# Performance work log

Hardware: AMD Instinct MI355X
Metric: run time of the kernel (lower is better)

## Reference

```python
import jax, jax.numpy as jnp
import numpy as np

B, S, I, H = 16, 4096, 256, 256
H_CYCLES, L_CYCLES = 2, 3


def setup_inputs() -> dict:
    key = jax.random.key(0)
    ks = jax.random.split(key, 18)
    g = lambda k, shape, s=0.05: jax.random.normal(k, shape, dtype=jnp.float32) * s
    return {
        "x": g(ks[0], (B, S, I), 1.0),
        "h0": jnp.zeros((1, B, H), jnp.float32),
        # GRU (PyTorch layout: rows ordered [reset, update, new])
        "gru_w_ih": g(ks[1], (3 * H, I)),
        "gru_w_hh": g(ks[2], (3 * H, H)),
        "gru_b_ih": g(ks[3], (3 * H,)),
        "gru_b_hh": g(ks[4], (3 * H,)),
        # L refine cell
        "Lg_w": g(ks[5], (H, 2 * H)), "Lg_b": g(ks[6], (H,)),
        "Lt_w": g(ks[7], (H, 2 * H)), "Lt_b": g(ks[8], (H,)),
        "Lu_w": g(ks[9], (H, H)),     "Lu_b": g(ks[10], (H,)),
        # H refine cell
        "Hg_w": g(ks[11], (H, 2 * H)), "Hg_b": g(ks[12], (H,)),
        "Ht_w": g(ks[13], (H, 2 * H)), "Ht_b": g(ks[14], (H,)),
        "Hu_w": g(ks[15], (H, H)),     "Hu_b": g(ks[16], (H,)),
    }


def _refine_cell(prev, hid, gw, gb, tw, tb, uw, ub):
    c = jnp.concatenate([prev, hid], axis=-1)            # (B, 2H)
    gate = jax.nn.sigmoid(c @ gw.T + gb)
    refinement = jnp.tanh(c @ tw.T + tb)
    out = gate * refinement + (1.0 - gate) * prev
    new_hid = jnp.tanh(out @ uw.T + ub)
    return out, new_hid


def reference(x, h0, gru_w_ih, gru_w_hh, gru_b_ih, gru_b_hh,
              Lg_w, Lg_b, Lt_w, Lt_b, Lu_w, Lu_b,
              Hg_w, Hg_b, Ht_w, Ht_b, Hu_w, Hu_b):
    # ---- GRU (single layer, batch_first), PyTorch gate equations ----
    x_proj = x @ gru_w_ih.T + gru_b_ih                   # (B, S, 3H)

    def gru_step(h, xp):
        hp = h @ gru_w_hh.T + gru_b_hh                   # (B, 3H)
        xr, xz, xn = jnp.split(xp, 3, axis=-1)
        hr, hz, hn = jnp.split(hp, 3, axis=-1)
        r = jax.nn.sigmoid(xr + hr)
        z = jax.nn.sigmoid(xz + hz)
        n = jnp.tanh(xn + r * hn)
        h_new = (1.0 - z) * n + z * h
        return h_new, h_new

    h_last, base_out = jax.lax.scan(gru_step, h0[0], x_proj.transpose(1, 0, 2))
    # base_out: (S, B, H)

    # ---- hierarchical recursive refinement; zH/zL persist across t ----
    def refine_step(carry, out_t):
        zH, zL = carry
        o = out_t
        for _ in range(H_CYCLES):
            for _ in range(L_CYCLES):
                o, zL = _refine_cell(o, zH, Lg_w, Lg_b, Lt_w, Lt_b, Lu_w, Lu_b)
            o, zH = _refine_cell(o, zL, Hg_w, Hg_b, Ht_w, Ht_b, Hu_w, Hu_b)
        return (zH, zL), o

    z0 = jnp.zeros((x.shape[0], H), x.dtype)
    _, refined = jax.lax.scan(refine_step, (z0, z0), base_out)  # (S, B, H)
    output = refined.transpose(1, 0, 2)                  # (B, S, H)
    return output, h_last[None]                          # hidden: (1, B, H)
```

## Files before the change

### kernel.cpp

```cpp
#include <hip/hip_runtime.h>
#include <math.h>


#define NB   16
#define SEQ  4096
#define TEAMS 8
#define WPT  32
#define BPT  2
#define NTH  256

typedef unsigned long long u64;
typedef unsigned u32x4 __attribute__((ext_vector_type(4)));

__device__ __forceinline__ float fexp(float v){ return __builtin_amdgcn_exp2f(v*1.44269504089f); }
__device__ __forceinline__ float sigf(float v){ return __builtin_amdgcn_rcpf(1.f + fexp(-v)); }
__device__ __forceinline__ float ftanh(float v){ return 2.f*sigf(2.f*v) - 1.f; }

__device__ __forceinline__ void swpw(u64* p, u64 v){
  (void)__hip_atomic_exchange(p, v, __ATOMIC_RELAXED, __HIP_MEMORY_SCOPE_AGENT);
}
__device__ __forceinline__ u64 ldw(const u64* p){
  return __hip_atomic_load(p, __ATOMIC_RELAXED, __HIP_MEMORY_SCOPE_AGENT);
}

typedef _Float16 h2f __attribute__((ext_vector_type(2)));
typedef __fp16   h2p __attribute__((ext_vector_type(2)));
union H2U { h2f f; h2p p; unsigned u; };
__device__ __forceinline__ unsigned pk2(float lo, float hi){
  H2U t; t.p = __builtin_amdgcn_cvt_pkrtz(lo, hi); return t.u;
}
__device__ __forceinline__ float2 upk2(unsigned w){
  H2U t; t.u = w; float2 r; r.x = (float)t.f.x; r.y = (float)t.f.y; return r;
}
__device__ __forceinline__ u64 packh(float lo, float hi, unsigned tag){
  return ((u64)tag<<32) | (u64)pk2(lo, hi);
}

__device__ __forceinline__ void poll2x(const u64* p, unsigned tag,
                                       unsigned &lo0, unsigned &lo1){
  u32x4 v;
  for(;;){
    asm volatile("global_load_dwordx4 %0, %1, off sc0 sc1\n\ts_waitcnt vmcnt(0)"
                 : "=&v"(v) : "v"(p) : "memory");
    if (v.y >= tag && v.w >= tag) break;
    __builtin_amdgcn_s_sleep(1);
  }
  lo0 = v.x; lo1 = v.z;
}

#define WGBAR() asm volatile("s_waitcnt lgkmcnt(0)\n\ts_barrier" ::: "memory")

extern "C" __global__ __launch_bounds__(NTH, 1)
void trm_kernel(const float* __restrict__ x,   const float* __restrict__ h0,
                const float* __restrict__ wih, const float* __restrict__ whh,
                const float* __restrict__ bih, const float* __restrict__ bhh,
                const float* __restrict__ Lgw, const float* __restrict__ Lgb,
                const float* __restrict__ Ltw, const float* __restrict__ Ltb,
                const float* __restrict__ Luw, const float* __restrict__ Lub,
                const float* __restrict__ Hgw, const float* __restrict__ Hgb,
                const float* __restrict__ Htw, const float* __restrict__ Htb,
                const float* __restrict__ Huw, const float* __restrict__ Hub,
                float* __restrict__ out, u64* __restrict__ act_base)
{
  const int team = blockIdx.x & (TEAMS-1);
  const int j    = blockIdx.x / TEAMS;
  const int tid  = threadIdx.x;

  __shared__ float wgRZ[16][520];
  __shared__ float wgX[8][264];
  __shared__ float wgN[8][264];
  __shared__ float wclG[8][520], wclT[8][520];
  __shared__ float wchG[8][520], wchT[8][520];
  __shared__ float wul[8][264],  wuh[8][264];
  __shared__ float xst [BPT][256];
  __shared__ float st_o [BPT][256];
  __shared__ float st_zh[BPT][256];
  __shared__ float st_zl[BPT][256];
  __shared__ float st_h [BPT][256];
  __shared__ float exvA[16][2], exvC[16][2], exvD[16][2];
  __shared__ float bR[8],bZ[8],bX[8],bN[8],bCLg[8],bCLt[8],bCHg[8],bCHt[8],bUL[8],bUH[8];

  {
    const int k = tid;
    for (int r=0;r<8;r++){
      const int nr = j*8+r;
      wgRZ[r][k]       = wih[(size_t)nr*256+k];
      wgRZ[r][256+k]   = whh[(size_t)nr*256+k];
      wgRZ[8+r][k]     = wih[(size_t)(256+nr)*256+k];
      wgRZ[8+r][256+k] = whh[(size_t)(256+nr)*256+k];
      wgX[r][k] = wih[(size_t)(512+nr)*256+k];
      wgN[r][k] = whh[(size_t)(512+nr)*256+k];
      wclG[r][k] = Lgw[(size_t)nr*512+k];  wclG[r][256+k] = Lgw[(size_t)nr*512+256+k];
      wclT[r][k] = Ltw[(size_t)nr*512+k];  wclT[r][256+k] = Ltw[(size_t)nr*512+256+k];
      wchG[r][k] = Hgw[(size_t)nr*512+k];  wchG[r][256+k] = Hgw[(size_t)nr*512+256+k];
      wchT[r][k] = Htw[(size_t)nr*512+k];  wchT[r][256+k] = Htw[(size_t)nr*512+256+k];
      wul[r][k] = Luw[(size_t)nr*256+k];
      wuh[r][k] = Huw[(size_t)nr*256+k];
    }
    if (tid<8){
      const int nr = j*8+tid;
      bR[tid]  = bih[nr]     + bhh[nr];
      bZ[tid]  = bih[256+nr] + bhh[256+nr];
      bX[tid]  = bih[512+nr];
      bN[tid]  = bhh[512+nr];
      bCLg[tid]= Lgb[nr];  bCLt[tid]= Ltb[nr];
      bCHg[tid]= Hgb[nr];  bCHt[tid]= Htb[nr];
      bUL[tid] = Lub[nr];  bUH[tid] = Hub[nr];
    }
    st_h[0][tid]  = h0[(team*BPT+0)*256+tid];
    st_h[1][tid]  = h0[(team*BPT+1)*256+tid];
    st_o[0][tid]  = 0.f;  st_o[1][tid]  = 0.f;
    st_zh[0][tid] = 0.f;  st_zh[1][tid] = 0.f;
    st_zl[0][tid] = 0.f;  st_zl[1][tid] = 0.f;
    xst[0][tid] = x[((size_t)(team*BPT+0)*SEQ + 0)*256 + tid];
    xst[1][tid] = x[((size_t)(team*BPT+1)*SEQ + 0)*256 + tid];
  }
  __syncthreads();

  u64* actT = act_base + (size_t)team*4096;
  u64* gb   = actT + 2048;
  unsigned kst = 0;
  const bool wr0 = (j == 0);

  auto gru_produce = [&](int step){
    const unsigned gt = (unsigned)step + 1u;
    u64* g = gb + (size_t)(step & 1)*512;
    const int u = tid>>4, kk = tid&15, r = u&7;
    {
      const float* wr = wgRZ[u];
      float a0=0.f, a1=0.f;
      #pragma unroll
      for (int i=0;i<16;i++){
        const float w = wr[kk+16*i];
        a0 += w*xst[0][kk+16*i];
        a1 += w*xst[1][kk+16*i];
      }
      #pragma unroll
      for (int i=0;i<16;i++){
        const float w = wr[256+kk+16*i];
        a0 += w*st_h[0][kk+16*i];
        a1 += w*st_h[1][kk+16*i];
      }
      a0 += __shfl_xor(a0,1); a0 += __shfl_xor(a0,2); a0 += __shfl_xor(a0,4); a0 += __shfl_xor(a0,8);
      a1 += __shfl_xor(a1,1); a1 += __shfl_xor(a1,2); a1 += __shfl_xor(a1,4); a1 += __shfl_xor(a1,8);
      if (kk==0){ exvC[u][0] = a0; exvC[u][1] = a1; }
    }
    {
      const bool isH = (u>=8);
      const float* wr = isH? wgN[r] : wgX[r];
      float (*src)[256] = isH? st_h : xst;
      float a0=0.f, a1=0.f;
      #pragma unroll
      for (int i=0;i<16;i++){
        const float w = wr[kk+16*i];
        a0 += w*src[0][kk+16*i];
        a1 += w*src[1][kk+16*i];
      }
      a0 += __shfl_xor(a0,1); a0 += __shfl_xor(a0,2); a0 += __shfl_xor(a0,4); a0 += __shfl_xor(a0,8);
      a1 += __shfl_xor(a1,1); a1 += __shfl_xor(a1,2); a1 += __shfl_xor(a1,4); a1 += __shfl_xor(a1,8);
      if (kk==0){ exvD[u][0] = a0; exvD[u][1] = a1; }
    }
    WGBAR();
    if (tid < 16){
      const int b = tid&1, rr = tid>>1;
      const float pr = exvC[rr][b]   + bR[rr];
      const float pz = exvC[8+rr][b] + bZ[rr];
      const float xn = exvD[rr][b]   + bX[rr];
      const float hn = exvD[8+rr][b] + bN[rr];
      const float rg = sigf(pr);
      const float zg = sigf(pz);
      const float ng = ftanh(xn + rg*hn);
      swpw(&g[(size_t)(j*8+rr)*2 + b], packh(ng, zg, gt));
    }
  };

  auto cstage = [&](float (*WG)[520], float (*WT)[520], float* bG, float* bT,
                    float (*hid)[256], bool wout, bool pg, int tt){
    const unsigned tag = kst + 1u;
    u64* buf = actT + (kst & 1u)*1024;
    WGBAR();
    const int u = tid>>4, kk = tid&15, r = u&7;
    const bool isT = (u>=8);
    const float* wr = isT? WT[r] : WG[r];
    float a0=0.f, a1=0.f;
    #pragma unroll
    for (int i=0;i<16;i++){
      const float w = wr[kk+16*i];
      a0 += w*st_o[0][kk+16*i];
      a1 += w*st_o[1][kk+16*i];
    }
    #pragma unroll
    for (int i=0;i<16;i++){
      const float w = wr[256+kk+16*i];
      a0 += w*hid[0][kk+16*i];
      a1 += w*hid[1][kk+16*i];
    }
    a0 += __shfl_xor(a0,1); a0 += __shfl_xor(a0,2); a0 += __shfl_xor(a0,4); a0 += __shfl_xor(a0,8);
    a1 += __shfl_xor(a1,1); a1 += __shfl_xor(a1,2); a1 += __shfl_xor(a1,4); a1 += __shfl_xor(a1,8);
    if (kk==0){ exvA[u][0] = a0; exvA[u][1] = a1; }
    WGBAR();
    if (tid < 16){
      const int b = tid&1, rr = tid>>1;
      const float g = sigf (exvA[rr][b]   + bG[rr]);
      const float T = ftanh(exvA[8+rr][b] + bT[rr]);
      swpw(&buf[(size_t)(j*8+rr)*2 + b], packh(g, T, tag));
    }
    if (pg) gru_produce(tt+1);
    unsigned lo0, lo1;
    poll2x(&buf[2*tid], tag, lo0, lo1);
    const float2 gt0 = upk2(lo0);
    const float2 gt1 = upk2(lo1);
    const float o0 = gt0.x*gt0.y + (1.f-gt0.x)*st_o[0][tid];
    const float o1 = gt1.x*gt1.y + (1.f-gt1.x)*st_o[1][tid];
    st_o[0][tid] = o0;
    st_o[1][tid] = o1;
    if (wout && wr0){
      out[((size_t)(team*BPT+0)*SEQ + tt)*256 + tid] = o0;
      out[((size_t)(team*BPT+1)*SEQ + tt)*256 + tid] = o1;
    }
    kst++;
  };

  auto ustage = [&](float (*W)[264], float* bU, float (*dst)[256]){
    const unsigned tag = kst + 1u;
    u64* buf = actT + (kst & 1u)*1024;
    WGBAR();
    const int u = tid>>5, kk = tid&31;
    const float* wr = W[u];
    float a0=0.f, a1=0.f;
    #pragma unroll
    for (int i=0;i<8;i++){
      const float w = wr[kk+32*i];
      a0 += w*st_o[0][kk+32*i];
      a1 += w*st_o[1][kk+32*i];
    }
    a0 += __shfl_xor(a0,1); a0 += __shfl_xor(a0,2); a0 += __shfl_xor(a0,4); a0 += __shfl_xor(a0,8); a0 += __shfl_xor(a0,16);
    a1 += __shfl_xor(a1,1); a1 += __shfl_xor(a1,2); a1 += __shfl_xor(a1,4); a1 += __shfl_xor(a1,8); a1 += __shfl_xor(a1,16);
    if (kk==0){ exvA[u][0] = a0; exvA[u][1] = a1; }
    WGBAR();
    if (tid < 8){
      const float v0 = ftanh(exvA[tid][0] + bU[tid]);
      const float v1 = ftanh(exvA[tid][1] + bU[tid]);
      swpw(&buf[j*8 + tid], packh(v0, v1, tag));
    }
    u64 w0;
    for(;;){
      w0 = ldw(&buf[tid]);
      if ((unsigned)(w0>>32) >= tag) break;
      __builtin_amdgcn_s_sleep(1);
    }
    const float2 v = upk2((unsigned)w0);
    dst[0][tid] = v.x;
    dst[1][tid] = v.y;
    kst++;
  };

  float px0 = x[((size_t)(team*BPT+0)*SEQ + 1)*256 + tid];
  float px1 = x[((size_t)(team*BPT+1)*SEQ + 1)*256 + tid];
  gru_produce(0);

  #pragma unroll 1
  for (int t=0; t<SEQ; ++t){
    {
      WGBAR();
      u64* g = gb + (size_t)(t & 1)*512;
      unsigned lo0, lo1;
      poll2x(&g[2*tid], (unsigned)(t+1), lo0, lo1);
      const float2 nz0 = upk2(lo0);
      const float2 nz1 = upk2(lo1);
      const float h0v = (1.f-nz0.y)*nz0.x + nz0.y*st_h[0][tid];
      const float h1v = (1.f-nz1.y)*nz1.x + nz1.y*st_h[1][tid];
      st_h[0][tid] = h0v;  st_o[0][tid] = h0v;
      st_h[1][tid] = h1v;  st_o[1][tid] = h1v;
      xst[0][tid] = px0;
      xst[1][tid] = px1;
      if (t+2 < SEQ){
        px0 = x[((size_t)(team*BPT+0)*SEQ + (t+2))*256 + tid];
        px1 = x[((size_t)(team*BPT+1)*SEQ + (t+2))*256 + tid];
      }
      if (t == SEQ-1 && wr0){
        out[(size_t)NB*SEQ*256 + (team*BPT+0)*256 + tid] = h0v;
        out[(size_t)NB*SEQ*256 + (team*BPT+1)*256 + tid] = h1v;
      }
    }
    #pragma unroll 1
    for (int c=0;c<2;c++){
      cstage(wclG,wclT,bCLg,bCLt,st_zh,false,(c==0)&&(t+1<SEQ),t);
      cstage(wclG,wclT,bCLg,bCLt,st_zh,false,false,t);
      cstage(wclG,wclT,bCLg,bCLt,st_zh,false,false,t);
      ustage(wul,bUL,st_zl);
      cstage(wchG,wchT,bCHg,bCHt,st_zl,(c==1),false,t);
      ustage(wuh,bUH,st_zh);
    }
  }
}

extern "C" void kernel_launch(void* const* d_in, const int* in_sizes, int n_in,
                              void* d_out, int out_size, void* d_ws, size_t ws_size,
                              hipStream_t stream)
{
  (void)hipMemsetAsync(d_ws, 0, (size_t)TEAMS*4096*sizeof(u64), stream);
  u64* act = (u64*)d_ws;

  dim3 grid(TEAMS*WPT), block(NTH);
  hipLaunchKernelGGL(trm_kernel, grid, block, 0, stream,
    (const float*)d_in[0],  (const float*)d_in[1],
    (const float*)d_in[2],  (const float*)d_in[3],
    (const float*)d_in[4],  (const float*)d_in[5],
    (const float*)d_in[6],  (const float*)d_in[7],
    (const float*)d_in[8],  (const float*)d_in[9],
    (const float*)d_in[10], (const float*)d_in[11],
    (const float*)d_in[12], (const float*)d_in[13],
    (const float*)d_in[14], (const float*)d_in[15],
    (const float*)d_in[16], (const float*)d_in[17],
    (float*)d_out, act);
}
```

Before: 87.04 ms.

## Interleave gate rows to finish activations in-wave and drop LDS exchange barriers

Reorders the GRU and refine-cell weight rows so each gate pair (r/z, x-new/h-new, gate/transform) sits in adjacent 16-lane groups of the same wavefront. The partner value is then fetched with a shfl_xor across 16 lanes, and lane kk==0 computes the activations and publishes them directly. This removes the shared-memory staging arrays and one workgroup barrier per stage on the latency-bound serial recurrence. In exchange, activation work moves onto 16 lanes per wave, each doing both batch elements, instead of a single 16-thread group.

Measured after the change: 141.9 ms. +63.0%, slower.

```diff
diff --git a/kernel.cpp b/kernel.cpp
--- a/kernel.cpp
+++ b/kernel.cpp
@@ -77,17 +77,16 @@
   __shared__ float st_zh[BPT][256];
   __shared__ float st_zl[BPT][256];
   __shared__ float st_h [BPT][256];
-  __shared__ float exvA[16][2], exvC[16][2], exvD[16][2];
   __shared__ float bR[8],bZ[8],bX[8],bN[8],bCLg[8],bCLt[8],bCHg[8],bCHt[8],bUL[8],bUH[8];
 
   {
     const int k = tid;
     for (int r=0;r<8;r++){
       const int nr = j*8+r;
-      wgRZ[r][k]       = wih[(size_t)nr*256+k];
-      wgRZ[r][256+k]   = whh[(size_t)nr*256+k];
-      wgRZ[8+r][k]     = wih[(size_t)(256+nr)*256+k];
-      wgRZ[8+r][256+k] = whh[(size_t)(256+nr)*256+k];
+      wgRZ[2*r][k]       = wih[(size_t)nr*256+k];
+      wgRZ[2*r][256+k]   = whh[(size_t)nr*256+k];
+      wgRZ[2*r+1][k]     = wih[(size_t)(256+nr)*256+k];
+      wgRZ[2*r+1][256+k] = whh[(size_t)(256+nr)*256+k];
       wgX[r][k] = wih[(size_t)(512+nr)*256+k];
       wgN[r][k] = whh[(size_t)(512+nr)*256+k];
       wclG[r][k] = Lgw[(size_t)nr*512+k];  wclG[r][256+k] = Lgw[(size_t)nr*512+256+k];
@@ -125,10 +124,11 @@
   auto gru_produce = [&](int step){
     const unsigned gt = (unsigned)step + 1u;
     u64* g = gb + (size_t)(step & 1)*512;
-    const int u = tid>>4, kk = tid&15, r = u&7;
+    const int u = tid>>4, kk = tid&15, r = u>>1;
+    const bool odd = (u&1);
+    float a0=0.f, a1=0.f;
     {
       const float* wr = wgRZ[u];
-      float a0=0.f, a1=0.f;
       #pragma unroll
       for (int i=0;i<16;i++){
         const float w = wr[kk+16*i];
@@ -143,34 +143,32 @@
       }
       a0 += __shfl_xor(a0,1); a0 += __shfl_xor(a0,2); a0 += __shfl_xor(a0,4); a0 += __shfl_xor(a0,8);
       a1 += __shfl_xor(a1,1); a1 += __shfl_xor(a1,2); a1 += __shfl_xor(a1,4); a1 += __shfl_xor(a1,8);
-      if (kk==0){ exvC[u][0] = a0; exvC[u][1] = a1; }
-    }
+    }
+    float c0=0.f, c1=0.f;
     {
-      const bool isH = (u>=8);
-      const float* wr = isH? wgN[r] : wgX[r];
-      float (*src)[256] = isH? st_h : xst;
-      float a0=0.f, a1=0.f;
+      const float* wr = odd? wgN[r] : wgX[r];
+      float (*src)[256] = odd? st_h : xst;
       #pragma unroll
       for (int i=0;i<16;i++){
         const float w = wr[kk+16*i];
-        a0 += w*src[0][kk+16*i];
-        a1 += w*src[1][kk+16*i];
-      }
-      a0 += __shfl_xor(a0,1); a0 += __shfl_xor(a0,2); a0 += __shfl_xor(a0,4); a0 += __shfl_xor(a0,8);
-      a1 += __shfl_xor(a1,1); a1 += __shfl_xor(a1,2); a1 += __shfl_xor(a1,4); a1 += __shfl_xor(a1,8);
-      if (kk==0){ exvD[u][0] = a0; exvD[u][1] = a1; }
-    }
-    WGBAR();
-    if (tid < 16){
-      const int b = tid&1, rr = tid>>1;
-      const float pr = exvC[rr][b]   + bR[rr];
-      const float pz = exvC[8+rr][b] + bZ[rr];
-      const float xn = exvD[rr][b]   + bX[rr];
-      const float hn = exvD[8+rr][b] + bN[rr];
-      const float rg = sigf(pr);
-      const float zg = sigf(pz);
-      const float ng = ftanh(xn + rg*hn);
-      swpw(&g[(size_t)(j*8+rr)*2 + b], packh(ng, zg, gt));
+        c0 += w*src[0][kk+16*i];
+        c1 += w*src[1][kk+16*i];
+      }
+      c0 += __shfl_xor(c0,1); c0 += __shfl_xor(c0,2); c0 += __shfl_xor(c0,4); c0 += __shfl_xor(c0,8);
+      c1 += __shfl_xor(c1,1); c1 += __shfl_xor(c1,2); c1 += __shfl_xor(c1,4); c1 += __shfl_xor(c1,8);
+    }
+    const float ta0 = __shfl_xor(a0,16), ta1 = __shfl_xor(a1,16);
+    const float tc0 = __shfl_xor(c0,16), tc1 = __shfl_xor(c1,16);
+    if (!odd && kk==0){
+      const float rg0 = sigf(a0 + bR[r]);
+      const float zg0 = sigf(ta0 + bZ[r]);
+      const float ng0 = ftanh(c0 + bX[r] + rg0*(tc0 + bN[r]));
+      const float rg1 = sigf(a1 + bR[r]);
+      const float zg1 = sigf(ta1 + bZ[r]);
+      const float ng1 = ftanh(c1 + bX[r] + rg1*(tc1 + bN[r]));
+      const int n = j*8+r;
+      swpw(&g[(size_t)n*2 + 0], packh(ng0, zg0, gt));
+      swpw(&g[(size_t)n*2 + 1], packh(ng1, zg1, gt));
     }
   };
 
@@ -179,8 +177,8 @@
     const unsigned tag = kst + 1u;
     u64* buf = actT + (kst & 1u)*1024;
     WGBAR();
-    const int u = tid>>4, kk = tid&15, r = u&7;
-    const bool isT = (u>=8);
+    const int u = tid>>4, kk = tid&15, r = u>>1;
+    const bool isT = (u&1);
     const float* wr = isT? WT[r] : WG[r];
     float a0=0.f, a1=0.f;
     #pragma unroll
@@ -197,13 +195,16 @@
     }
     a0 += __shfl_xor(a0,1); a0 += __shfl_xor(a0,2); a0 += __shfl_xor(a0,4); a0 += __shfl_xor(a0,8);
     a1 += __shfl_xor(a1,1); a1 += __shfl_xor(a1,2); a1 += __shfl_xor(a1,4); a1 += __shfl_xor(a1,8);
-    if (kk==0){ exvA[u][0] = a0; exvA[u][1] = a1; }
-    WGBAR();
-    if (tid < 16){
-      const int b = tid&1, rr = tid>>1;
-      const float g = sigf (exvA[rr][b]   + bG[rr]);
-      const float T = ftanh(exvA[8+rr][b] + bT[rr]);
-      swpw(&buf[(size_t)(j*8+rr)*2 + b], packh(g, T, tag));
+    const float t0 = __shfl_xor(a0,16);
+    const float t1 = __shfl_xor(a1,16);
+    if (!isT && kk==0){
+      const float g0 = sigf (a0 + bG[r]);
+      const float T0 = ftanh(t0 + bT[r]);
+      const float g1 = sigf (a1 + bG[r]);
+      const float T1 = ftanh(t1 + bT[r]);
+      const int n = j*8+r;
+      swpw(&buf[(size_t)n*2 + 0], packh(g0, T0, tag));
+      swpw(&buf[(size_t)n*2 + 1], packh(g1, T1, tag));
     }
     if (pg) gru_produce(tt+1);
     unsigned lo0, lo1;
@@ -236,12 +237,10 @@
     }
     a0 += __shfl_xor(a0,1); a0 += __shfl_xor(a0,2); a0 += __shfl_xor(a0,4); a0 += __shfl_xor(a0,8); a0 += __shfl_xor(a0,16);
     a1 += __shfl_xor(a1,1); a1 += __shfl_xor(a1,2); a1 += __shfl_xor(a1,4); a1 += __shfl_xor(a1,8); a1 += __shfl_xor(a1,16);
-    if (kk==0){ exvA[u][0] = a0; exvA[u][1] = a1; }
-    WGBAR();
-    if (tid < 8){
-      const float v0 = ftanh(exvA[tid][0] + bU[tid]);
-      const float v1 = ftanh(exvA[tid][1] + bU[tid]);
-      swpw(&buf[j*8 + tid], packh(v0, v1, tag));
+    if (kk==0){
+      const float v0 = ftanh(a0 + bU[u]);
+      const float v1 = ftanh(a1 + bU[u]);
+      swpw(&buf[j*8 + u], packh(v0, v1, tag));
     }
     u64 w0;
     for(;;){
```

## Use workgroup-scope atomics when a team's workgroups share one XCC

Applied to the files above, without the earlier changes.

At startup each workgroup publishes its XCC id to a flag array. A team whose 32 workgroups all sit on the same XCC switches to a fast path that uses workgroup-scope exchanges for publishing and fetch_add(0) reads for polling, with no sleep in the poll loops. The aim is to cut the latency of the cross-workgroup handoffs that serialize every refinement stage. This relies on all members of a team landing on one XCC, which the default placement may not do, and on workgroup-scope atomics being coherent through a shared L2. It also adds a startup handshake and spin loops that never sleep.

After: 86.04 ms. No clear change (-1.1%).

```diff
diff --git a/kernel.cpp b/kernel.cpp
--- a/kernel.cpp
+++ b/kernel.cpp
@@ -16,11 +16,22 @@
 __device__ __forceinline__ float sigf(float v){ return __builtin_amdgcn_rcpf(1.f + fexp(-v)); }
 __device__ __forceinline__ float ftanh(float v){ return 2.f*sigf(2.f*v) - 1.f; }
 
-__device__ __forceinline__ void swpw(u64* p, u64 v){
-  (void)__hip_atomic_exchange(p, v, __ATOMIC_RELAXED, __HIP_MEMORY_SCOPE_AGENT);
+__device__ __forceinline__ void st_ag(unsigned* p, unsigned v){
+  __hip_atomic_store(p, v, __ATOMIC_RELAXED, __HIP_MEMORY_SCOPE_AGENT);
+}
+__device__ __forceinline__ unsigned ld_ag(const unsigned* p){
+  return __hip_atomic_load(p, __ATOMIC_RELAXED, __HIP_MEMORY_SCOPE_AGENT);
+}
+
+__device__ __forceinline__ void swpw(u64* p, u64 v, bool fast){
+  if (fast) (void)__hip_atomic_exchange(p, v, __ATOMIC_RELAXED, __HIP_MEMORY_SCOPE_WORKGROUP);
+  else      (void)__hip_atomic_exchange(p, v, __ATOMIC_RELAXED, __HIP_MEMORY_SCOPE_AGENT);
 }
 __device__ __forceinline__ u64 ldw(const u64* p){
   return __hip_atomic_load(p, __ATOMIC_RELAXED, __HIP_MEMORY_SCOPE_AGENT);
+}
+__device__ __forceinline__ u64 rmw(u64* p){
+  return __hip_atomic_fetch_add(p, 0ull, __ATOMIC_RELAXED, __HIP_MEMORY_SCOPE_WORKGROUP);
 }
 
 typedef _Float16 h2f __attribute__((ext_vector_type(2)));
@@ -36,16 +47,47 @@
   return ((u64)tag<<32) | (u64)pk2(lo, hi);
 }
 
-__device__ __forceinline__ void poll2x(const u64* p, unsigned tag,
+__device__ __forceinline__ void poll2x(u64* p, unsigned tag, bool fast,
                                        unsigned &lo0, unsigned &lo1){
-  u32x4 v;
-  for(;;){
-    asm volatile("global_load_dwordx4 %0, %1, off sc0 sc1\n\ts_waitcnt vmcnt(0)"
-                 : "=&v"(v) : "v"(p) : "memory");
-    if (v.y >= tag && v.w >= tag) break;
-    __builtin_amdgcn_s_sleep(1);
-  }
-  lo0 = v.x; lo1 = v.z;
+  if (fast){
+    for(;;){
+      u64 w0 = rmw(p);
+      u64 w1 = rmw(p+1);
+      if ((unsigned)(w0>>32) >= tag && (unsigned)(w1>>32) >= tag){
+        lo0 = (unsigned)w0; lo1 = (unsigned)w1; return;
+      }
+      u32x4 v;
+      asm volatile("global_load_dwordx4 %0, %1, off sc0 sc1\n\ts_waitcnt vmcnt(0)"
+                   : "=&v"(v) : "v"(p) : "memory");
+      if (v.y >= tag && v.w >= tag){ lo0 = v.x; lo1 = v.z; return; }
+    }
+  } else {
+    u32x4 v;
+    for(;;){
+      asm volatile("global_load_dwordx4 %0, %1, off sc0 sc1\n\ts_waitcnt vmcnt(0)"
+                   : "=&v"(v) : "v"(p) : "memory");
+      if (v.y >= tag && v.w >= tag) break;
+      __builtin_amdgcn_s_sleep(1);
+    }
+    lo0 = v.x; lo1 = v.z;
+  }
+}
+
+__device__ __forceinline__ unsigned poll1x(u64* p, unsigned tag, bool fast){
+  if (fast){
+    for(;;){
+      u64 w = rmw(p);
+      if ((unsigned)(w>>32) >= tag) return (unsigned)w;
+      w = ldw(p);
+      if ((unsigned)(w>>32) >= tag) return (unsigned)w;
+    }
+  } else {
+    for(;;){
+      u64 w = ldw(p);
+      if ((unsigned)(w>>32) >= tag) return (unsigned)w;
+      __builtin_amdgcn_s_sleep(1);
+    }
+  }
 }
 
 #define WGBAR() asm volatile("s_waitcnt lgkmcnt(0)\n\ts_barrier" ::: "memory")
@@ -60,7 +102,8 @@
                 const float* __restrict__ Hgw, const float* __restrict__ Hgb,
                 const float* __restrict__ Htw, const float* __restrict__ Htb,
                 const float* __restrict__ Huw, const float* __restrict__ Hub,
-                float* __restrict__ out, u64* __restrict__ act_base)
+                float* __restrict__ out,
+                unsigned* __restrict__ flg_base, u64* __restrict__ act_base)
 {
   const int team = blockIdx.x & (TEAMS-1);
   const int j    = blockIdx.x / TEAMS;
@@ -115,7 +158,27 @@
     xst[0][tid] = x[((size_t)(team*BPT+0)*SEQ + 0)*256 + tid];
     xst[1][tid] = x[((size_t)(team*BPT+1)*SEQ + 0)*256 + tid];
   }
+
+  unsigned* flg = flg_base + team*1024;
+  unsigned xcc = 0;
+  asm volatile("s_getreg_b32 %0, hwreg(HW_REG_XCC_ID)" : "=s"(xcc));
   __syncthreads();
+  if (tid == 0) st_ag(flg + j, 0x100u | xcc);
+  if (tid < 64){
+    const int fl = tid & 31;
+    for (;;){
+      unsigned v = ld_ag(flg + fl);
+      if (__all(v != 0)) break;
+      __builtin_amdgcn_s_sleep(8);
+    }
+  }
+  __syncthreads();
+  bool fast;
+  {
+    unsigned v  = ld_ag(flg + (tid & 31));
+    unsigned v0 = __shfl(v, 0);
+    fast = __all(v == v0);
+  }
 
   u64* actT = act_base + (size_t)team*4096;
   u64* gb   = actT + 2048;
@@ -170,7 +233,7 @@
       const float rg = sigf(pr);
       const float zg = sigf(pz);
       const float ng = ftanh(xn + rg*hn);
-      swpw(&g[(size_t)(j*8+rr)*2 + b], packh(ng, zg, gt));
+      swpw(&g[(size_t)(j*8+rr)*2 + b], packh(ng, zg, gt), fast);
     }
   };
 
@@ -203,11 +266,11 @@
       const int b = tid&1, rr = tid>>1;
       const float g = sigf (exvA[rr][b]   + bG[rr]);
       const float T = ftanh(exvA[8+rr][b] + bT[rr]);
-      swpw(&buf[(size_t)(j*8+rr)*2 + b], packh(g, T, tag));
+      swpw(&buf[(size_t)(j*8+rr)*2 + b], packh(g, T, tag), fast);
     }
     if (pg) gru_produce(tt+1);
     unsigned lo0, lo1;
-    poll2x(&buf[2*tid], tag, lo0, lo1);
+    poll2x(&buf[2*tid], tag, fast, lo0, lo1);
     const float2 gt0 = upk2(lo0);
     const float2 gt1 = upk2(lo1);
     const float o0 = gt0.x*gt0.y + (1.f-gt0.x)*st_o[0][tid];
@@ -241,15 +304,10 @@
     if (tid < 8){
       const float v0 = ftanh(exvA[tid][0] + bU[tid]);
       const float v1 = ftanh(exvA[tid][1] + bU[tid]);
-      swpw(&buf[j*8 + tid], packh(v0, v1, tag));
-    }
-    u64 w0;
-    for(;;){
-      w0 = ldw(&buf[tid]);
-      if ((unsigned)(w0>>32) >= tag) break;
-      __builtin_amdgcn_s_sleep(1);
-    }
-    const float2 v = upk2((unsigned)w0);
+      swpw(&buf[j*8 + tid], packh(v0, v1, tag), fast);
+    }
+    const unsigned lo = poll1x(&buf[tid], tag, fast);
+    const float2 v = upk2(lo);
     dst[0][tid] = v.x;
     dst[1][tid] = v.y;
     kst++;
@@ -265,7 +323,7 @@
       WGBAR();
       u64* g = gb + (size_t)(t & 1)*512;
       unsigned lo0, lo1;
-      poll2x(&g[2*tid], (unsigned)(t+1), lo0, lo1);
+      poll2x(&g[2*tid], (unsigned)(t+1), fast, lo0, lo1);
       const float2 nz0 = upk2(lo0);
       const float2 nz1 = upk2(lo1);
       const float h0v = (1.f-nz0.y)*nz0.x + nz0.y*st_h[0][tid];
@@ -299,8 +357,9 @@
                               void* d_out, int out_size, void* d_ws, size_t ws_size,
                               hipStream_t stream)
 {
-  (void)hipMemsetAsync(d_ws, 0, (size_t)TEAMS*4096*sizeof(u64), stream);
-  u64* act = (u64*)d_ws;
+  (void)hipMemsetAsync(d_ws, 0, 65536 + (size_t)TEAMS*4096*sizeof(u64), stream);
+  unsigned* flg = (unsigned*)d_ws;
+  u64* act = (u64*)((char*)d_ws + 65536);
 
   dim3 grid(TEAMS*WPT), block(NTH);
   hipLaunchKernelGGL(trm_kernel, grid, block, 0, stream,
@@ -313,5 +372,5 @@
     (const float*)d_in[12], (const float*)d_in[13],
     (const float*)d_in[14], (const float*)d_in[15],
     (const float*)d_in[16], (const float*)d_in[17],
-    (float*)d_out, act);
-}
+    (float*)d_out, flg, act);
+}
```
